# Performance work log

Hardware: AMD Instinct MI355X
Metric: run time of the kernel (lower is better)

The kernel has to match this reference:

```python
import jax, jax.numpy as jnp
import numpy as np

N, M, D = 16384, 1024, 1024


def setup_inputs() -> dict:
    key = jax.random.key(0)
    kq, kp = jax.random.split(key)
    query = jax.random.normal(kq, (N, D), dtype=jnp.float32)
    proto = jax.random.normal(kp, (M, D), dtype=jnp.float32)
    return {"query": query, "proto": proto}


def reference(query, proto):
    # Pairwise squared euclidean: ||q||^2 - 2 q.p + ||p||^2  (same math as
    # the expand+pow+sum in compute_euclidean, but without the [N,M,D] blowup).
    q2 = jnp.sum(query * query, axis=-1, keepdims=True)          # [N,1]
    p2 = jnp.sum(proto * proto, axis=-1)                          # [M]
    qp = jnp.einsum('nd,md->nm', query, proto)                    # [N,M]
    dists = q2 - 2.0 * qp + p2[None, :]                           # [N,M]
    # Original applies F.softmax(-dists, dim=1) (named log_p_y but is softmax).
    return jax.nn.softmax(-dists, axis=1)
```

## Files before the change

### kernel.cpp

```cpp
#include <hip/hip_runtime.h>
#include <stdint.h>

#define N_Q 16384
#define M_P 1024
#define D_K 1024

typedef __attribute__((ext_vector_type(8))) __bf16 bf16x8;
typedef __attribute__((ext_vector_type(4))) float floatx4;
typedef __attribute__((ext_vector_type(4))) unsigned int uint4v;

#define AS1 __attribute__((address_space(1)))
#define AS3 __attribute__((address_space(3)))

__device__ __forceinline__ unsigned short f2bf(float f) {
    unsigned int u = __float_as_uint(f);
    u += 0x7fffu + ((u >> 16) & 1u);
    return (unsigned short)(u >> 16);
}
__device__ __forceinline__ float bf2f(unsigned short h) {
    return __uint_as_float(((unsigned int)h) << 16);
}

__device__ __forceinline__ void split_chunk(floatx4 f0, floatx4 f1,
                                            uint4v* hi, uint4v* lo) {
    float e[8] = {f0.x, f0.y, f0.z, f0.w, f1.x, f1.y, f1.z, f1.w};
    unsigned int hb[4], lb[4];
#pragma unroll
    for (int p = 0; p < 4; ++p) {
        unsigned int u0 = __float_as_uint(e[2 * p]);
        unsigned int u1 = __float_as_uint(e[2 * p + 1]);
        hb[p] = __builtin_amdgcn_perm(u1, u0, 0x07060302);
        float l0 = e[2 * p]     - __uint_as_float(u0 & 0xffff0000u);
        float l1 = e[2 * p + 1] - __uint_as_float(u1 & 0xffff0000u);
        lb[p] = __builtin_amdgcn_perm(__float_as_uint(l1), __float_as_uint(l0),
                                      0x07060302);
    }
    uint4v h = {hb[0], hb[1], hb[2], hb[3]};
    uint4v l = {lb[0], lb[1], lb[2], lb[3]};
    *hi = h;
    *lo = l;
}

__global__ __launch_bounds__(256) void convert_proto_kernel(
    const float* __restrict__ proto, unsigned short* __restrict__ ph,
    unsigned short* __restrict__ pl, float* __restrict__ p2) {
    __shared__ float sred[4];
    int m = blockIdx.x;
    int t = threadIdx.x;
    size_t base4 = (size_t)m * (D_K / 4) + t;
    float4 v = ((const float4*)proto)[base4];
    ushort4 h, l;
    h.x = f2bf(v.x); l.x = f2bf(v.x - bf2f(h.x));
    h.y = f2bf(v.y); l.y = f2bf(v.y - bf2f(h.y));
    h.z = f2bf(v.z); l.z = f2bf(v.z - bf2f(h.z));
    h.w = f2bf(v.w); l.w = f2bf(v.w - bf2f(h.w));
    ((ushort4*)ph)[base4] = h;
    ((ushort4*)pl)[base4] = l;
    float sq = v.x * v.x + v.y * v.y + v.z * v.z + v.w * v.w;
#pragma unroll
    for (int off = 1; off < 64; off <<= 1) sq += __shfl_xor(sq, off);
    if ((t & 63) == 0) sred[t >> 6] = sq;
    __syncthreads();
    if (t == 0) p2[m] = sred[0] + sred[1] + sred[2] + sred[3];
}

__global__ __launch_bounds__(512, 2) void gemm_logits_kernel(
    const float* __restrict__ query,
    const unsigned short* __restrict__ ph, const unsigned short* __restrict__ pl,
    const float* __restrict__ p2, float* __restrict__ out) {
    __shared__ unsigned short sAh[2][16 * 512];
    __shared__ unsigned short sAl[2][16 * 512];
    __shared__ unsigned short sBh[2][16 * 512];
    __shared__ unsigned short sBl[2][16 * 512];

    const int tid = threadIdx.x;
    const int wave = tid >> 6;
    const int lane = tid & 63;
    const int wr = wave >> 2;
    const int wc = wave & 3;

    const int b = blockIdx.x;
    const int v = (b & 7) * 32 + (b >> 3);
    const int colt = v >> 6;
    const int rowt = v & 63;
    const int row0 = rowt * 256;
    const int col0 = colt * 256;

    const int rlB = lane >> 2;
    const int cioB = (lane & 3) ^ ((lane >> 3) & 3);
    const int halfB = wave >> 2;
    const int sgB = wave & 3;
    const unsigned short* gB = (halfB ? pl : ph)
        + (size_t)(col0 + sgB * 64 + rlB) * D_K + cioB * 8;

    const int rlA = lane >> 2;
    const int cA = lane & 3;
    const AS1 float* gA = (const AS1 float*)query
        + (size_t)(row0 + wave * 32 + rlA) * D_K + cA * 8;
    const int wroff = (4 * rlA + (cA ^ ((rlA >> 1) & 3))) * 8;

    const int rsel = lane & 15;
    const int kq = lane >> 4;
    const int fragoff = (4 * rsel + (kq ^ ((rsel >> 1) & 3))) * 8;

    floatx4 zero = {0.0f, 0.0f, 0.0f, 0.0f};
    floatx4 acc[8][4];
#pragma unroll
    for (int i = 0; i < 8; ++i)
#pragma unroll
        for (int j = 0; j < 4; ++j) acc[i][j] = zero;

    floatx4 f0[2], f1[2];
    bf16x8 bh[4], bl[4];
    bf16x8 ah[2][2], al[2][2];

    auto issueA = [&](int kb) {
#pragma unroll
        for (int s = 0; s < 2; ++s) {
            const AS1 float* p = gA + (size_t)(s * 16) * D_K + kb;
            f0[s] = *(const AS1 floatx4*)p;
            f1[s] = *(const AS1 floatx4*)(p + 4);
        }
    };
    auto issueB = [&](int kb, int nxt) {
        unsigned short* dstB = (halfB ? sBl[nxt] : sBh[nxt]) + sgB * 4 * 512;
#pragma unroll
        for (int s = 0; s < 4; ++s)
            __builtin_amdgcn_global_load_lds(
                (const AS1 unsigned int*)(const void*)(gB + (size_t)(s * 16) * D_K + kb),
                (AS3 unsigned int*)(void*)(dstB + s * 512), 16, 0, 0);
    };
    auto writeA = [&](int nxt, int s) {
        uint4v hi, lo;
        split_chunk(f0[s], f1[s], &hi, &lo);
        const int off = (wave * 2 + s) * 512 + wroff;
        *(uint4v*)(sAh[nxt] + off) = hi;
        *(uint4v*)(sAl[nxt] + off) = lo;
    };
    auto ldBfrag = [&](int cur) {
#pragma unroll
        for (int j = 0; j < 4; ++j) {
            const int boff = (wc * 4 + j) * 512 + fragoff;
            bh[j] = *(const bf16x8*)(sBh[cur] + boff);
            bl[j] = *(const bf16x8*)(sBl[cur] + boff);
        }
    };
    auto ldA = [&](int cur, int i0, int set) {
#pragma unroll
        for (int t = 0; t < 2; ++t) {
            const int aoff = (wr * 8 + i0 + t) * 512 + fragoff;
            ah[set][t] = *(const bf16x8*)(sAh[cur] + aoff);
            al[set][t] = *(const bf16x8*)(sAl[cur] + aoff);
        }
    };
    auto mfma2 = [&](int i0, int set) {
#pragma unroll
        for (int j = 0; j < 4; ++j)
#pragma unroll
            for (int t = 0; t < 2; ++t) {
                acc[i0 + t][j] = __builtin_amdgcn_mfma_f32_16x16x32_bf16(ah[set][t], bh[j], acc[i0 + t][j], 0, 0, 0);
                acc[i0 + t][j] = __builtin_amdgcn_mfma_f32_16x16x32_bf16(ah[set][t], bl[j], acc[i0 + t][j], 0, 0, 0);
                acc[i0 + t][j] = __builtin_amdgcn_mfma_f32_16x16x32_bf16(al[set][t], bh[j], acc[i0 + t][j], 0, 0, 0);
            }
    };

#define LGKM_MFMA(n, i0, set)                                   \
    asm volatile("s_waitcnt lgkmcnt(" #n ")" ::: "memory");     \
    __builtin_amdgcn_sched_barrier(0);                          \
    __builtin_amdgcn_s_setprio(1);                              \
    mfma2(i0, set);                                             \
    __builtin_amdgcn_s_setprio(0);

    auto stepf = [&](int kbnB, int kbnA, int cur, int nxt, bool pfB, bool pfA) {
        if (pfB) issueB(kbnB, nxt);
        ldBfrag(cur);
        ldA(cur, 0, 0);
        ldA(cur, 2, 1);
        LGKM_MFMA(4, 0, 0)
        ldA(cur, 4, 0);
        LGKM_MFMA(4, 2, 1)
        ldA(cur, 6, 1);
        LGKM_MFMA(4, 4, 0)
        if (pfB) { writeA(nxt, 0); writeA(nxt, 1); }
        if (pfA) issueA(kbnA);
        asm volatile("s_waitcnt lgkmcnt(0)" ::: "memory");
        if (pfB) {
            if (pfA) asm volatile("s_waitcnt vmcnt(4)" ::: "memory");
            else     asm volatile("s_waitcnt vmcnt(0)" ::: "memory");
        }
        __builtin_amdgcn_sched_barrier(0);
        __builtin_amdgcn_s_setprio(1);
        mfma2(6, 1);
        __builtin_amdgcn_s_setprio(0);
        __builtin_amdgcn_s_barrier();
    };

    issueA(0);
    issueB(0, 0);
    writeA(0, 0);
    writeA(0, 1);
    issueA(32);
    asm volatile("s_waitcnt lgkmcnt(0)" ::: "memory");
    asm volatile("s_waitcnt vmcnt(4)" ::: "memory");
    __builtin_amdgcn_s_barrier();

    for (int kt = 0; kt < 30; kt += 2) {
        stepf((kt + 1) * 32, (kt + 2) * 32, 0, 1, true, true);
        stepf((kt + 2) * 32, (kt + 3) * 32, 1, 0, true, true);
    }
    stepf(31 * 32, 0, 0, 1, true, false);
    stepf(0, 0, 1, 0, false, false);

#undef LGKM_MFMA

#pragma unroll
    for (int j = 0; j < 4; ++j) {
        const int gc = col0 + wc * 64 + j * 16 + rsel;
        const float p2v = p2[gc];
#pragma unroll
        for (int i = 0; i < 8; ++i) {
            const int gr = row0 + wr * 128 + i * 16 + kq * 4;
#pragma unroll
            for (int r = 0; r < 4; ++r) {
                out[(size_t)(gr + r) * M_P + gc] = 2.0f * acc[i][j][r] - p2v;
            }
        }
    }
}

__global__ __launch_bounds__(256) void naive_logits_kernel(
    const float* __restrict__ query, const float* __restrict__ proto,
    float* __restrict__ out) {
    __shared__ float qs[D_K];
    int n = blockIdx.x;
    int t = threadIdx.x;
    ((float4*)qs)[t] = ((const float4*)(query + (size_t)n * D_K))[t];
    __syncthreads();
    float acc[4] = {0.f, 0.f, 0.f, 0.f};
    float pp[4] = {0.f, 0.f, 0.f, 0.f};
    for (int d = 0; d < D_K; d += 4) {
        float4 qv = *(const float4*)(qs + d);
#pragma unroll
        for (int j = 0; j < 4; ++j) {
            const float4 pv = *(const float4*)(proto + (size_t)(t + 256 * j) * D_K + d);
            acc[j] += qv.x * pv.x + qv.y * pv.y + qv.z * pv.z + qv.w * pv.w;
            pp[j] += pv.x * pv.x + pv.y * pv.y + pv.z * pv.z + pv.w * pv.w;
        }
    }
#pragma unroll
    for (int j = 0; j < 4; ++j)
        out[(size_t)n * M_P + t + 256 * j] = 2.0f * acc[j] - pp[j];
}

__global__ __launch_bounds__(256) void softmax_kernel(float* __restrict__ out) {
    const int lane = threadIdx.x & 63;
    int n = blockIdx.x * 4 + (threadIdx.x >> 6);
    for (int it = 0; it < 2; ++it, n += 8192) {
        float* row = out + (size_t)n * M_P;
        floatx4 v[4];
#pragma unroll
        for (int k = 0; k < 4; ++k)
            v[k] = *((const floatx4*)row + k * 64 + lane);
        float mx = fmaxf(fmaxf(v[0].x, v[0].y), fmaxf(v[0].z, v[0].w));
#pragma unroll
        for (int k = 1; k < 4; ++k)
            mx = fmaxf(mx, fmaxf(fmaxf(v[k].x, v[k].y), fmaxf(v[k].z, v[k].w)));
#pragma unroll
        for (int off = 1; off < 64; off <<= 1) mx = fmaxf(mx, __shfl_xor(mx, off));
        float s = 0.0f;
#pragma unroll
        for (int k = 0; k < 4; ++k) {
            v[k].x = __expf(v[k].x - mx);
            v[k].y = __expf(v[k].y - mx);
            v[k].z = __expf(v[k].z - mx);
            v[k].w = __expf(v[k].w - mx);
            s += v[k].x + v[k].y + v[k].z + v[k].w;
        }
#pragma unroll
        for (int off = 1; off < 64; off <<= 1) s += __shfl_xor(s, off);
        const float inv = 1.0f / s;
#pragma unroll
        for (int k = 0; k < 4; ++k) {
            floatx4 o;
            o.x = v[k].x * inv; o.y = v[k].y * inv;
            o.z = v[k].z * inv; o.w = v[k].w * inv;
            __builtin_nontemporal_store(o, (floatx4*)row + k * 64 + lane);
        }
    }
}

extern "C" void kernel_launch(void* const* d_in, const int* in_sizes, int n_in,
                              void* d_out, int out_size, void* d_ws, size_t ws_size,
                              hipStream_t stream) {
    const float* query = (const float*)d_in[0];
    const float* proto = (const float*)d_in[1];
    float* out = (float*)d_out;

    const size_t pElems = (size_t)M_P * D_K;
    const size_t needed = pElems * 2 * 2 + M_P * 4;

    if (ws_size >= needed) {
        unsigned short* ph = (unsigned short*)d_ws;
        unsigned short* pl = ph + pElems;
        float* p2 = (float*)(pl + pElems);

        convert_proto_kernel<<<M_P, 256, 0, stream>>>(proto, ph, pl, p2);
        gemm_logits_kernel<<<(N_Q / 256) * (M_P / 256), 512, 0, stream>>>(
            query, ph, pl, p2, out);
    } else {
        naive_logits_kernel<<<N_Q, 256, 0, stream>>>(query, proto, out);
    }
    softmax_kernel<<<2048, 256, 0, stream>>>(out);
}
```

Baseline: 198.1 us.

## Shrink GEMM block tile to 128x128 with more blocks and occupancy

Reduces the per-block output tile from 256x256 to 128x128, giving each wave a 64x32 sub-tile. Shared buffers, register arrays, load counts and waitcnt values are resized to match. The workgroup raster swizzle is dropped, and launch bounds now target 4 blocks per CU. The aim is more blocks and higher occupancy to hide latency, at the cost of lower arithmetic intensity and more global and LDS traffic per FLOP.

```diff
diff --git a/kernel.cpp b/kernel.cpp
--- a/kernel.cpp
+++ b/kernel.cpp
@@ -64,14 +64,14 @@
     if (t == 0) p2[m] = sred[0] + sred[1] + sred[2] + sred[3];
 }
 
-__global__ __launch_bounds__(512, 2) void gemm_logits_kernel(
+__global__ __launch_bounds__(512, 4) void gemm_logits_kernel(
     const float* __restrict__ query,
     const unsigned short* __restrict__ ph, const unsigned short* __restrict__ pl,
     const float* __restrict__ p2, float* __restrict__ out) {
-    __shared__ unsigned short sAh[2][16 * 512];
-    __shared__ unsigned short sAl[2][16 * 512];
-    __shared__ unsigned short sBh[2][16 * 512];
-    __shared__ unsigned short sBl[2][16 * 512];
+    __shared__ unsigned short sAh[2][8 * 512];
+    __shared__ unsigned short sAl[2][8 * 512];
+    __shared__ unsigned short sBh[2][8 * 512];
+    __shared__ unsigned short sBl[2][8 * 512];
 
     const int tid = threadIdx.x;
     const int wave = tid >> 6;
@@ -80,23 +80,22 @@
     const int wc = wave & 3;
 
     const int b = blockIdx.x;
-    const int v = (b & 7) * 32 + (b >> 3);
-    const int colt = v >> 6;
-    const int rowt = v & 63;
-    const int row0 = rowt * 256;
-    const int col0 = colt * 256;
+    const int colt = b & 7;
+    const int rowt = b >> 3;
+    const int row0 = rowt * 128;
+    const int col0 = colt * 128;
 
     const int rlB = lane >> 2;
     const int cioB = (lane & 3) ^ ((lane >> 3) & 3);
     const int halfB = wave >> 2;
     const int sgB = wave & 3;
     const unsigned short* gB = (halfB ? pl : ph)
-        + (size_t)(col0 + sgB * 64 + rlB) * D_K + cioB * 8;
+        + (size_t)(col0 + sgB * 32 + rlB) * D_K + cioB * 8;
 
     const int rlA = lane >> 2;
     const int cA = lane & 3;
     const AS1 float* gA = (const AS1 float*)query
-        + (size_t)(row0 + wave * 32 + rlA) * D_K + cA * 8;
+        + (size_t)(row0 + wave * 16 + rlA) * D_K + cA * 8;
     const int wroff = (4 * rlA + (cA ^ ((rlA >> 1) & 3))) * 8;
 
     const int rsel = lane & 15;
@@ -104,104 +103,97 @@
     const int fragoff = (4 * rsel + (kq ^ ((rsel >> 1) & 3))) * 8;
 
     floatx4 zero = {0.0f, 0.0f, 0.0f, 0.0f};
-    floatx4 acc[8][4];
-#pragma unroll
-    for (int i = 0; i < 8; ++i)
-#pragma unroll
-        for (int j = 0; j < 4; ++j) acc[i][j] = zero;
-
-    floatx4 f0[2], f1[2];
-    bf16x8 bh[4], bl[4];
-    bf16x8 ah[2][2], al[2][2];
+    floatx4 acc[4][2];
+#pragma unroll
+    for (int i = 0; i < 4; ++i)
+#pragma unroll
+        for (int j = 0; j < 2; ++j) acc[i][j] = zero;
+
+    floatx4 f0, f1;
+    bf16x8 bh[2], bl[2];
+    bf16x8 ah[2], al[2];
 
     auto issueA = [&](int kb) {
-#pragma unroll
-        for (int s = 0; s < 2; ++s) {
-            const AS1 float* p = gA + (size_t)(s * 16) * D_K + kb;
-            f0[s] = *(const AS1 floatx4*)p;
-            f1[s] = *(const AS1 floatx4*)(p + 4);
-        }
+        const AS1 float* p = gA + kb;
+        f0 = *(const AS1 floatx4*)p;
+        f1 = *(const AS1 floatx4*)(p + 4);
     };
     auto issueB = [&](int kb, int nxt) {
-        unsigned short* dstB = (halfB ? sBl[nxt] : sBh[nxt]) + sgB * 4 * 512;
-#pragma unroll
-        for (int s = 0; s < 4; ++s)
+        unsigned short* dstB = (halfB ? sBl[nxt] : sBh[nxt]) + sgB * 2 * 512;
+#pragma unroll
+        for (int s = 0; s < 2; ++s)
             __builtin_amdgcn_global_load_lds(
                 (const AS1 unsigned int*)(const void*)(gB + (size_t)(s * 16) * D_K + kb),
                 (AS3 unsigned int*)(void*)(dstB + s * 512), 16, 0, 0);
     };
-    auto writeA = [&](int nxt, int s) {
+    auto writeA = [&](int nxt) {
         uint4v hi, lo;
-        split_chunk(f0[s], f1[s], &hi, &lo);
-        const int off = (wave * 2 + s) * 512 + wroff;
+        split_chunk(f0, f1, &hi, &lo);
+        const int off = wave * 512 + wroff;
         *(uint4v*)(sAh[nxt] + off) = hi;
         *(uint4v*)(sAl[nxt] + off) = lo;
     };
     auto ldBfrag = [&](int cur) {
 #pragma unroll
-        for (int j = 0; j < 4; ++j) {
-            const int boff = (wc * 4 + j) * 512 + fragoff;
+        for (int j = 0; j < 2; ++j) {
+            const int boff = (wc * 2 + j) * 512 + fragoff;
             bh[j] = *(const bf16x8*)(sBh[cur] + boff);
             bl[j] = *(const bf16x8*)(sBl[cur] + boff);
         }
     };
-    auto ldA = [&](int cur, int i0, int set) {
-#pragma unroll
-        for (int t = 0; t < 2; ++t) {
-            const int aoff = (wr * 8 + i0 + t) * 512 + fragoff;
-            ah[set][t] = *(const bf16x8*)(sAh[cur] + aoff);
-            al[set][t] = *(const bf16x8*)(sAl[cur] + aoff);
-        }
-    };
-    auto mfma2 = [&](int i0, int set) {
-#pragma unroll
-        for (int j = 0; j < 4; ++j)
-#pragma unroll
-            for (int t = 0; t < 2; ++t) {
-                acc[i0 + t][j] = __builtin_amdgcn_mfma_f32_16x16x32_bf16(ah[set][t], bh[j], acc[i0 + t][j], 0, 0, 0);
-                acc[i0 + t][j] = __builtin_amdgcn_mfma_f32_16x16x32_bf16(ah[set][t], bl[j], acc[i0 + t][j], 0, 0, 0);
-                acc[i0 + t][j] = __builtin_amdgcn_mfma_f32_16x16x32_bf16(al[set][t], bh[j], acc[i0 + t][j], 0, 0, 0);
-            }
-    };
-
-#define LGKM_MFMA(n, i0, set)                                   \
+    auto ldA = [&](int cur, int i, int set) {
+        const int aoff = (wr * 4 + i) * 512 + fragoff;
+        ah[set] = *(const bf16x8*)(sAh[cur] + aoff);
+        al[set] = *(const bf16x8*)(sAl[cur] + aoff);
+    };
+    auto mfmaC = [&](int i, int set) {
+#pragma unroll
+        for (int j = 0; j < 2; ++j) {
+            acc[i][j] = __builtin_amdgcn_mfma_f32_16x16x32_bf16(ah[set], bh[j], acc[i][j], 0, 0, 0);
+            acc[i][j] = __builtin_amdgcn_mfma_f32_16x16x32_bf16(ah[set], bl[j], acc[i][j], 0, 0, 0);
+            acc[i][j] = __builtin_amdgcn_mfma_f32_16x16x32_bf16(al[set], bh[j], acc[i][j], 0, 0, 0);
+        }
+    };
+
+#define LGKM_MFMA(n, i, set)                                    \
     asm volatile("s_waitcnt lgkmcnt(" #n ")" ::: "memory");     \
     __builtin_amdgcn_sched_barrier(0);                          \
     __builtin_amdgcn_s_setprio(1);                              \
-    mfma2(i0, set);                                             \
+    mfmaC(i, set);                                              \
     __builtin_amdgcn_s_setprio(0);
 
-    auto stepf = [&](int kbnB, int kbnA, int cur, int nxt, bool pfB, bool pfA) {
-        if (pfB) issueB(kbnB, nxt);
+    auto stepf = [&](int kbB, int kbA, int cur, int nxt, bool pfB, bool pfA) {
+        if (pfB) issueB(kbB, nxt);
         ldBfrag(cur);
         ldA(cur, 0, 0);
-        ldA(cur, 2, 1);
-        LGKM_MFMA(4, 0, 0)
-        ldA(cur, 4, 0);
-        LGKM_MFMA(4, 2, 1)
-        ldA(cur, 6, 1);
-        LGKM_MFMA(4, 4, 0)
-        if (pfB) { writeA(nxt, 0); writeA(nxt, 1); }
-        if (pfA) issueA(kbnA);
+        ldA(cur, 1, 1);
+        LGKM_MFMA(2, 0, 0)
+        ldA(cur, 2, 0);
+        LGKM_MFMA(2, 1, 1)
+        ldA(cur, 3, 1);
+        LGKM_MFMA(2, 2, 0)
+        if (pfB) writeA(nxt);
+        if (pfA) issueA(kbA);
+        if (pfB) { asm volatile("s_waitcnt lgkmcnt(2)" ::: "memory"); }
+        else     { asm volatile("s_waitcnt lgkmcnt(0)" ::: "memory"); }
+        __builtin_amdgcn_sched_barrier(0);
+        __builtin_amdgcn_s_setprio(1);
+        mfmaC(3, 1);
+        __builtin_amdgcn_s_setprio(0);
         asm volatile("s_waitcnt lgkmcnt(0)" ::: "memory");
         if (pfB) {
-            if (pfA) asm volatile("s_waitcnt vmcnt(4)" ::: "memory");
-            else     asm volatile("s_waitcnt vmcnt(0)" ::: "memory");
-        }
-        __builtin_amdgcn_sched_barrier(0);
-        __builtin_amdgcn_s_setprio(1);
-        mfma2(6, 1);
-        __builtin_amdgcn_s_setprio(0);
+            if (pfA) { asm volatile("s_waitcnt vmcnt(2)" ::: "memory"); }
+            else     { asm volatile("s_waitcnt vmcnt(0)" ::: "memory"); }
+        }
         __builtin_amdgcn_s_barrier();
     };
 
     issueA(0);
     issueB(0, 0);
-    writeA(0, 0);
-    writeA(0, 1);
+    writeA(0);
     issueA(32);
     asm volatile("s_waitcnt lgkmcnt(0)" ::: "memory");
-    asm volatile("s_waitcnt vmcnt(4)" ::: "memory");
+    asm volatile("s_waitcnt vmcnt(2)" ::: "memory");
     __builtin_amdgcn_s_barrier();
 
     for (int kt = 0; kt < 30; kt += 2) {
@@ -214,12 +206,12 @@
 #undef LGKM_MFMA
 
 #pragma unroll
-    for (int j = 0; j < 4; ++j) {
-        const int gc = col0 + wc * 64 + j * 16 + rsel;
+    for (int j = 0; j < 2; ++j) {
+        const int gc = col0 + wc * 32 + j * 16 + rsel;
         const float p2v = p2[gc];
 #pragma unroll
-        for (int i = 0; i < 8; ++i) {
-            const int gr = row0 + wr * 128 + i * 16 + kq * 4;
+        for (int i = 0; i < 4; ++i) {
+            const int gr = row0 + wr * 64 + i * 16 + kq * 4;
 #pragma unroll
             for (int r = 0; r < 4; ++r) {
                 out[(size_t)(gr + r) * M_P + gc] = 2.0f * acc[i][j][r] - p2v;
@@ -305,7 +297,7 @@
         float* p2 = (float*)(pl + pElems);
 
         convert_proto_kernel<<<M_P, 256, 0, stream>>>(proto, ph, pl, p2);
-        gemm_logits_kernel<<<(N_Q / 256) * (M_P / 256), 512, 0, stream>>>(
+        gemm_logits_kernel<<<(N_Q / 128) * (M_P / 128), 512, 0, stream>>>(
             query, ph, pl, p2, out);
     } else {
         naive_logits_kernel<<<N_Q, 256, 0, stream>>>(query, proto, out);
```

Result: slower. 222.2 us (+12.2%).
